# Optimization experiments

Measured on AMD Instinct MI355X. Metric: run time of the kernel, lower is better.

## Reference

```python
import jax, jax.numpy as jnp
import numpy as np

NUM_OOV = 1000
NEG = -1e12


def _lstm_cell(x, h, c, Wx, Wh, b):
    # keras gate order: i, f, g(cell), o
    z = x @ Wx + h @ Wh + b
    i, f, g, o = jnp.split(z, 4, axis=-1)
    c = jax.nn.sigmoid(f) * c + jax.nn.sigmoid(i) * jnp.tanh(g)
    h = jax.nn.sigmoid(o) * jnp.tanh(c)
    return h, c


def setup_inputs() -> dict:
    key = jax.random.key(0)
    ks = jax.random.split(key, 16)
    B, T, S, V, E, H = 16, 100, 400, 50000, 128, 256
    rn = lambda k, shp, s=0.05: (jax.random.normal(k, shp) * s).astype(jnp.float32)
    return dict(
        trg_seq=jax.random.randint(ks[0], (B, T), 0, V),
        ext_src_seq=jax.random.randint(ks[1], (B, S), 0, V + NUM_OOV),
        encoder_mask=jax.random.randint(ks[2], (B, S), 0, 2).at[:, 0].set(1),
        encoder_outputs=rn(ks[3], (B, S, H), 1.0),
        init_h=rn(ks[4], (B, H)),
        init_c=rn(ks[5], (B, H)),
        emb=rn(ks[6], (V, E)),
        W_enc=rn(ks[7], (H, H)), b_enc=jnp.zeros((H,), jnp.float32),
        W_red=rn(ks[8], (E + H, E)), b_red=jnp.zeros((E,), jnp.float32),
        Wx=rn(ks[9], (E, 4 * H)), Wh=rn(ks[10], (H, 4 * H)), b_lstm=jnp.zeros((4 * H,), jnp.float32),
        W_cat=rn(ks[11], (2 * H, H)), b_cat=jnp.zeros((H,), jnp.float32),
        W_out=rn(ks[12], (H, V)), b_out=jnp.zeros((V,), jnp.float32),
    )


def reference(trg_seq, ext_src_seq, encoder_mask, encoder_outputs, init_h, init_c,
              emb, W_enc, b_enc, W_red, b_red, Wx, Wh, b_lstm, W_cat, b_cat, W_out, b_out):
    V = W_out.shape[1]
    B, S = ext_src_seq.shape
    EXT_V = V + NUM_OOV
    memories = encoder_outputs @ W_enc + b_enc              # [B,S,H]
    mask0 = encoder_mask == 0                               # [B,S]
    bidx = jnp.arange(B)[:, None]

    def step(carry, y_t):
        h, c, ctx = carry
        x = jnp.concatenate([emb[y_t], ctx], -1) @ W_red + b_red   # [B,E]
        h, c = _lstm_cell(x, h, c, Wx, Wh, b_lstm)
        energy = jnp.einsum('bh,bsh->bs', h, memories)
        energy = jnp.where(mask0, NEG, energy)
        attn = jax.nn.softmax(energy, axis=-1)
        ctx = jnp.einsum('bs,bsh->bh', attn, memories)
        logit = jnp.tanh(jnp.concatenate([h, ctx], -1) @ W_cat + b_cat) @ W_out + b_out  # [B,V]
        ext = jnp.concatenate([logit, jnp.zeros((B, NUM_OOV), logit.dtype)], -1)         # [B,EXT_V]
        # pointer-generator copy score: per-batch scatter-max of energy over extended ids
        copy = jnp.full((B, EXT_V), NEG, logit.dtype).at[bidx, ext_src_seq].max(energy)
        copy = jnp.where(copy < NEG / 2, 0.0, copy)
        return (h, c, ctx), ext + copy

    init = (init_h, init_c, jnp.zeros_like(init_h))
    _, logits = jax.lax.scan(step, init, trg_seq.T)          # [T,B,EXT_V]
    return jnp.transpose(logits, (1, 0, 2))                  # [B,T,EXT_V]
```

## Files before the change

kernel.cpp:

```cpp
#include <hip/hip_runtime.h>

#define DEV __device__ __forceinline__

#define B_    16
#define T_    100
#define S_    400
#define V_    50000
#define EXTV  51000
#define E_    128
#define H_    256
#define H4_   1024
#define NEG_  (-1e12f)
#define NWG_  80

DEV unsigned short f2bf(float x) {
    unsigned int u = __float_as_uint(x);
    u = (u + 0x7FFFu + ((u >> 16) & 1u)) >> 16;
    return (unsigned short)u;
}
DEV float sigm(float x) { return 1.f / (1.f + __expf(-x)); }

DEV float aload(const float* p) {
    return __uint_as_float(__hip_atomic_load((const unsigned int*)p,
                           __ATOMIC_RELAXED, __HIP_MEMORY_SCOPE_AGENT));
}
DEV void astore(float* p, float v) {
    __hip_atomic_store((unsigned int*)p, __float_as_uint(v),
                       __ATOMIC_RELAXED, __HIP_MEMORY_SCOPE_AGENT);
}

DEV void gbar(int* bar, int token) {
    __syncthreads();
    const int tid = threadIdx.x;
    int* gen = bar + 1344;
    if (blockIdx.x == 0) {
        if (tid >= 1 && tid < NWG_) {
            while (__hip_atomic_load(bar + tid * 16, __ATOMIC_RELAXED,
                                     __HIP_MEMORY_SCOPE_AGENT) < token)
                __builtin_amdgcn_s_sleep(2);
        }
        __syncthreads();
        if (tid == 0)
            __hip_atomic_store(gen, token, __ATOMIC_RELAXED, __HIP_MEMORY_SCOPE_AGENT);
    } else {
        if (tid == 0) {
            __hip_atomic_store(bar + blockIdx.x * 16, token,
                               __ATOMIC_RELAXED, __HIP_MEMORY_SCOPE_AGENT);
            while (__hip_atomic_load(gen, __ATOMIC_RELAXED,
                                     __HIP_MEMORY_SCOPE_AGENT) < token)
                __builtin_amdgcn_s_sleep(2);
        }
        __syncthreads();
    }
}

__global__ void k_init(int* bar) {
    for (int i = threadIdx.x; i < 2048; i += 256) bar[i] = 0;
}


__global__ void k_mem(const float* __restrict__ enc, const float* __restrict__ W_enc,
                      const float* __restrict__ b_enc, float* __restrict__ mem) {
    __shared__ float u[16][H_];
    int base = blockIdx.x * 16;
    int j = threadIdx.x;
    for (int r = 0; r < 16; ++r) u[r][j] = enc[(base + r) * H_ + j];
    __syncthreads();
    float acc[16];
    float bb = b_enc[j];
    for (int r = 0; r < 16; ++r) acc[r] = bb;
    for (int k = 0; k < H_; ++k) {
        float wv = W_enc[k * H_ + j];
        for (int r = 0; r < 16; ++r) acc[r] = fmaf(u[r][k], wv, acc[r]);
    }
    for (int r = 0; r < 16; ++r) mem[(base + r) * H_ + j] = acc[r];
}

__global__ void k_prepw(const float* __restrict__ W_red, const float* __restrict__ Wx,
                        const float* __restrict__ Wh, const float* __restrict__ b_red,
                        const float* __restrict__ b_lstm,
                        float* __restrict__ Kt, float* __restrict__ WtW, float* __restrict__ bvec) {
    int c = blockIdx.x * 256 + threadIdx.x;
    int r = blockIdx.y;
    if (r < 384) {
        float acc = 0.f;
        for (int j = 0; j < E_; ++j) acc = fmaf(W_red[r * E_ + j], Wx[j * H4_ + c], acc);
        if (r < 128) WtW[r * H4_ + c] = acc;
        else         Kt[c * 512 + (r - 128)] = acc;
    } else if (r < 640) {
        Kt[c * 512 + 256 + (r - 384)] = Wh[(r - 384) * H4_ + c];
    } else {
        float acc = b_lstm[c];
        for (int j = 0; j < E_; ++j) acc = fmaf(b_red[j], Wx[j * H4_ + c], acc);
        bvec[c] = acc;
    }
}

__global__ void k_zpre(const int* __restrict__ trg, const float* __restrict__ emb,
                       const float* __restrict__ WtW, const float* __restrict__ bvec,
                       float* __restrict__ Zpre) {
    __shared__ float u[16][E_];
    int t = blockIdx.x, q = blockIdx.y;
    int tid = threadIdx.x;
    for (int idx = tid; idx < 16 * E_; idx += 256) {
        int b = idx >> 7, k = idx & 127;
        u[b][k] = emb[trg[b * T_ + t] * E_ + k];
    }
    __syncthreads();
    int c = q * 256 + tid;
    float acc[16];
    float bv = bvec[c];
    for (int b = 0; b < 16; ++b) acc[b] = bv;
    for (int k = 0; k < E_; ++k) {
        float wv = WtW[k * H4_ + c];
        for (int b = 0; b < 16; ++b) acc[b] = fmaf(u[b][k], wv, acc[b]);
    }
    for (int b = 0; b < 16; ++b) Zpre[(t * 16 + b) * H4_ + c] = acc[b];
}

__global__ void __launch_bounds__(512) k_loop(
    const float* __restrict__ Kt, const float* __restrict__ Zpre,
    const float* __restrict__ init_h, const float* __restrict__ init_c,
    const float* __restrict__ memw, const int* __restrict__ enc_mask,
    float* __restrict__ Mpart, float* __restrict__ Zpart, float* __restrict__ Cpart,
    float* __restrict__ ws_h, float* __restrict__ ws_ctx, float* __restrict__ ws_en,
    int* bar) {
    __shared__ __align__(16) float Kl[16 * 512];
    __shared__ __align__(16) float vL[16 * 512];
    __shared__ float zscr[16 * 17];
    __shared__ float swL[80];
    __shared__ float invd[16];
    __shared__ float hA[H_];
    __shared__ float eL[80];
    __shared__ float pL[80];
    __shared__ float red1[1];
    __shared__ float cL[512];

    const int w = blockIdx.x, tid = threadIdx.x;
    const int ub = (w & 63) << 2;

    float c_state = 0.f;
    if (w < 64 && tid < 64)
        c_state = init_c[(tid & 15) * H_ + ub + (tid >> 4)];

    if (w < 64) {
        for (int idx = tid; idx < 16 * 512; idx += 512) {
            int cs = idx >> 9, k = idx & 511;
            int col = ((cs >> 2) << 8) + ub + (cs & 3);
            Kl[idx] = Kt[col * 512 + k];
        }
    }

    for (int t = 0; ; ++t) {
        const bool aw = (t == T_) ? (w < 16) : (w < 64);
        if (aw) {
            if (t == 0) {
                for (int idx = tid; idx < 4096; idx += 512) {
                    int b = idx >> 8, k = idx & 255;
                    vL[b * 512 + k] = 0.f;
                    vL[b * 512 + 256 + k] = init_h[b * H_ + k];
                }
            } else {
                if (tid < 16) {
                    int b = tid;
                    float m[5], zp[5];
                    float M = -3.0e38f;
                    for (int i = 0; i < 5; ++i) {
                        m[i] = aload(&Mpart[i * 16 + b]); zp[i] = aload(&Zpart[i * 16 + b]);
                        M = fmaxf(M, m[i]);
                    }
                    float den = 0.f;
                    for (int i = 0; i < 5; ++i) {
                        float s = __expf(m[i] - M);
                        swL[i * 16 + b] = s;
                        den = fmaf(zp[i], s, den);
                    }
                    invd[b] = 1.f / den;
                }
                __syncthreads();
                for (int idx = tid; idx < 4096; idx += 512) {
                    int b = idx >> 8, k = idx & 255;
                    float v = 0.f;
                    for (int i = 0; i < 5; ++i)
                        v = fmaf(aload(&Cpart[(i * 16 + b) * H_ + k]), swL[i * 16 + b], v);
                    v *= invd[b];
                    vL[b * 512 + k] = v;
                    if (w == b) ws_ctx[((t - 1) * 16 + b) * H_ + k] = v;
                    vL[b * 512 + 256 + k] = aload(&ws_h[((t - 1) * 16 + b) * H_ + k]);
                }
            }
        }
        if (t == T_) break;

        if (w < 64) {
            __syncthreads();
            const int wv = tid >> 6, kl = tid & 63, k0 = kl << 3;
            for (int pass = 0; pass < 2; ++pass) {
                const int cs = pass * 8 + wv;
                const float4 kv0 = *(const float4*)(Kl + cs * 512 + k0);
                const float4 kv1 = *(const float4*)(Kl + cs * 512 + k0 + 4);
                for (int b = 0; b < 16; ++b) {
                    float4 v0 = *(const float4*)(vL + b * 512 + k0);
                    float4 v1 = *(const float4*)(vL + b * 512 + k0 + 4);
                    float acc = v0.x * kv0.x;
                    acc = fmaf(v0.y, kv0.y, acc); acc = fmaf(v0.z, kv0.z, acc);
                    acc = fmaf(v0.w, kv0.w, acc); acc = fmaf(v1.x, kv1.x, acc);
                    acc = fmaf(v1.y, kv1.y, acc); acc = fmaf(v1.z, kv1.z, acc);
                    acc = fmaf(v1.w, kv1.w, acc);
                    for (int off = 32; off; off >>= 1) acc += __shfl_xor(acc, off);
                    if (kl == 0) zscr[cs * 17 + b] = acc;
                }
            }
            __syncthreads();
            if (tid < 64) {
                const int gu = tid >> 4, gb = tid & 15;
                const float* zp2 = Zpre + (t * 16 + gb) * H4_;
                float zi = zscr[gu * 17 + gb]        + zp2[ub + gu];
                float zf = zscr[(4 + gu) * 17 + gb]  + zp2[256 + ub + gu];
                float zg = zscr[(8 + gu) * 17 + gb]  + zp2[512 + ub + gu];
                float zo = zscr[(12 + gu) * 17 + gb] + zp2[768 + ub + gu];
                float cn = sigm(zf) * c_state + sigm(zi) * tanhf(zg);
                c_state = cn;
                astore(&ws_h[(t * 16 + gb) * H_ + ub + gu], sigm(zo) * tanhf(cn));
            }
        }
        gbar(bar, 2 * t + 1);

        {
            const int bw = w & 15, sg = w >> 4;
            if (tid < H_) hA[tid] = aload(&ws_h[(t * 16 + bw) * H_ + tid]);
            __syncthreads();
            if (tid < 320) {
                const int s = tid >> 2, kq = tid & 3;
                const float* mrow = memw + (bw * S_ + sg * 80 + s) * H_ + (kq << 6);
                const float* ha = hA + (kq << 6);
                float e = 0.f;
                for (int k = 0; k < 64; k += 4) {
                    float4 mm = *(const float4*)(mrow + k);
                    e = fmaf(ha[k], mm.x, e);     e = fmaf(ha[k + 1], mm.y, e);
                    e = fmaf(ha[k + 2], mm.z, e); e = fmaf(ha[k + 3], mm.w, e);
                }
                e += __shfl_xor(e, 1);
                e += __shfl_xor(e, 2);
                if (kq == 0) {
                    if (enc_mask[bw * S_ + sg * 80 + s] == 0) e = NEG_;
                    ws_en[(t * 16 + bw) * S_ + sg * 80 + s] = e;
                    eL[s] = e;
                }
            }
            __syncthreads();
            if (tid < 64) {
                float m = eL[tid];
                if (tid < 16) m = fmaxf(m, eL[64 + tid]);
                for (int off = 32; off; off >>= 1) m = fmaxf(m, __shfl_down(m, off));
                if (tid == 0) red1[0] = m;
            }
            __syncthreads();
            const float mw = red1[0];
            if (tid < 80) pL[tid] = __expf(eL[tid] - mw);
            __syncthreads();
            if (tid < 64) {
                float zz = pL[tid] + ((tid < 16) ? pL[64 + tid] : 0.f);
                for (int off = 32; off; off >>= 1) zz += __shfl_down(zz, off);
                if (tid == 0) { astore(&Mpart[sg * 16 + bw], mw); astore(&Zpart[sg * 16 + bw], zz); }
            }
            {
                const int k = tid & 255, half = tid >> 8;
                float acc = 0.f;
                const float* mbase = memw + (bw * S_ + sg * 80) * H_;
                for (int s = half * 40; s < half * 40 + 40; ++s)
                    acc = fmaf(pL[s], mbase[s * H_ + k], acc);
                cL[tid] = acc;
                __syncthreads();
                if (tid < 256) astore(&Cpart[(sg * 16 + bw) * H_ + tid], cL[tid] + cL[tid + 256]);
            }
        }
        gbar(bar, 2 * t + 2);
    }
}


__global__ void k_precat(const float* __restrict__ ws_h, const float* __restrict__ ws_ctx,
                         const float* __restrict__ W_cat, const float* __restrict__ b_cat,
                         unsigned short* __restrict__ Abf) {
    __shared__ float u[16][512];
    int base = blockIdx.x * 16;
    int tid = threadIdx.x;
    for (int idx = tid; idx < 16 * 512; idx += 256) {
        int r = idx >> 9, k = idx & 511;
        int row = base + r;
        float v = 0.f;
        if (row < 1600) v = (k < 256) ? ws_h[row * H_ + k] : ws_ctx[row * H_ + (k - 256)];
        u[r][k] = v;
    }
    __syncthreads();
    float acc[16];
    float bc = b_cat[tid];
    for (int r = 0; r < 16; ++r) acc[r] = bc;
    for (int k = 0; k < 512; ++k) {
        float wv = W_cat[k * H_ + tid];
        for (int r = 0; r < 16; ++r) acc[r] = fmaf(u[r][k], wv, acc[r]);
    }
    for (int r = 0; r < 16; ++r) {
        int row = base + r;
        float a = (row < 1600) ? tanhf(acc[r]) : 0.f;
        Abf[row * H_ + tid] = f2bf(a);
    }
}

__global__ void k_convw(const float* __restrict__ Wout, const float* __restrict__ bout,
                        unsigned short* __restrict__ Bt, float* __restrict__ biasp) {
    __shared__ float tile[64][65];
    int bx = blockIdx.x;
    int by = blockIdx.y;
    int tid = threadIdx.x;
    int tr = tid >> 6, tc = tid & 63;
    for (int i = 0; i < 16; ++i) {
        int k = by * 64 + tr + i * 4;
        int n = bx * 64 + tc;
        tile[tr + i * 4][tc] = (n < V_) ? Wout[k * V_ + n] : 0.f;
    }
    __syncthreads();
    for (int i = 0; i < 16; ++i) {
        int nl = tr + i * 4;
        int n = bx * 64 + nl;
        int k = by * 64 + tc;
        Bt[n * 256 + k] = f2bf(tile[tc][nl]);
    }
    if (by == 0 && tid < 64) {
        int n = bx * 64 + tid;
        biasp[n] = (n < V_) ? bout[n] : 0.f;
    }
}

typedef __attribute__((ext_vector_type(8))) __bf16 bf16x8;
typedef __attribute__((ext_vector_type(4))) float f32x4;

__global__ void __launch_bounds__(256) k_gemm(
    const unsigned short* __restrict__ A, const unsigned short* __restrict__ Bt,
    const float* __restrict__ biasp, float* __restrict__ out) {
    __shared__ __align__(16) unsigned short As[128 * 64];
    __shared__ __align__(16) unsigned short Bs[128 * 64];
    const int nb = blockIdx.x, mb = blockIdx.y;
    const int tid = threadIdx.x;
    const int lane = tid & 63, wv = tid >> 6;
    const int wm = wv >> 1, wn = wv & 1;
    const int q = lane >> 4, r16 = lane & 15;
    f32x4 acc[4][4];
    for (int i = 0; i < 4; ++i) for (int j = 0; j < 4; ++j) acc[i][j] = (f32x4)0.f;
    for (int kb = 0; kb < 4; ++kb) {
        for (int i = 0; i < 4; ++i) {
            int idx = tid + (i << 8);
            int m = idx >> 3, c = idx & 7;
            int sl = ((c ^ (m & 7)) << 3);
            *(uint4*)(As + (m << 6) + sl) = *(const uint4*)(A + (mb * 128 + m) * 256 + (kb << 6) + (c << 3));
            *(uint4*)(Bs + (m << 6) + sl) = *(const uint4*)(Bt + (nb * 128 + m) * 256 + (kb << 6) + (c << 3));
        }
        __syncthreads();
        for (int k32 = 0; k32 < 2; ++k32) {
            bf16x8 af[4], bfr[4];
            int c = (k32 << 2) + q;
            for (int mt = 0; mt < 4; ++mt) {
                int m = wm * 64 + mt * 16 + r16;
                af[mt] = *(const bf16x8*)(As + (m << 6) + ((c ^ (m & 7)) << 3));
            }
            for (int nt = 0; nt < 4; ++nt) {
                int n = wn * 64 + nt * 16 + r16;
                bfr[nt] = *(const bf16x8*)(Bs + (n << 6) + ((c ^ (n & 7)) << 3));
            }
            for (int mt = 0; mt < 4; ++mt)
                for (int nt = 0; nt < 4; ++nt)
                    acc[mt][nt] = __builtin_amdgcn_mfma_f32_16x16x32_bf16(af[mt], bfr[nt], acc[mt][nt], 0, 0, 0);
        }
        __syncthreads();
    }
    for (int nt = 0; nt < 4; ++nt) {
        int col = nb * 128 + wn * 64 + nt * 16 + r16;
        if (col >= EXTV) continue;
        float bs = biasp[col];
        for (int mt = 0; mt < 4; ++mt) {
            int rbase = mb * 128 + wm * 64 + mt * 16 + (q << 2);
            for (int rg = 0; rg < 4; ++rg) {
                int row = rbase + rg;
                if (row < 1600) {
                    int tt = row >> 4, bb = row & 15;
                    out[(bb * T_ + tt) * EXTV + col] = acc[mt][nt][rg] + bs;
                }
            }
        }
    }
}

__global__ void k_scatter(const int* __restrict__ ext_ids, const float* __restrict__ ws_en,
                          float* __restrict__ out) {
    __shared__ int ids[S_];
    __shared__ float en[S_];
    int r = blockIdx.x;
    int t = r >> 4, b = r & 15;
    int tid = threadIdx.x;
    for (int s = tid; s < S_; s += 256) {
        ids[s] = ext_ids[b * S_ + s];
        en[s] = ws_en[r * S_ + s];
    }
    __syncthreads();
    for (int s = tid; s < S_; s += 256) {
        int id = ids[s];
        float mx = en[s];
        int fo = s;
        for (int s2 = 0; s2 < S_; ++s2) {
            if (ids[s2] == id) { mx = fmaxf(mx, en[s2]); if (s2 < fo) fo = s2; }
        }
        if (fo == s && mx >= NEG_ * 0.5f)
            out[(b * T_ + t) * EXTV + id] += mx;
    }
}


extern "C" void kernel_launch(void* const* d_in, const int* in_sizes, int n_in,
                              void* d_out, int out_size, void* d_ws, size_t ws_size,
                              hipStream_t stream) {
    (void)in_sizes; (void)n_in; (void)out_size; (void)ws_size;
    const int*   trg     = (const int*)d_in[0];
    const int*   ext_ids = (const int*)d_in[1];
    const int*   mask    = (const int*)d_in[2];
    const float* enc     = (const float*)d_in[3];
    const float* init_h  = (const float*)d_in[4];
    const float* init_c  = (const float*)d_in[5];
    const float* emb     = (const float*)d_in[6];
    const float* W_enc   = (const float*)d_in[7];
    const float* b_enc   = (const float*)d_in[8];
    const float* W_red   = (const float*)d_in[9];
    const float* b_red   = (const float*)d_in[10];
    const float* Wx      = (const float*)d_in[11];
    const float* Wh      = (const float*)d_in[12];
    const float* b_lstm  = (const float*)d_in[13];
    const float* W_cat   = (const float*)d_in[14];
    const float* b_cat   = (const float*)d_in[15];
    const float* W_out   = (const float*)d_in[16];
    const float* b_out   = (const float*)d_in[17];
    float* out = (float*)d_out;

    char* p = (char*)d_ws;
    auto alloc = [&](size_t bytes) { char* r = p; p += ((bytes + 255) & ~size_t(255)); return r; };
    float* mem_w = (float*)alloc(1638400u * 4);
    float* Kt    = (float*)alloc(524288u * 4);
    float* WtW   = (float*)alloc(131072u * 4);
    float* bvec  = (float*)alloc(1024u * 4);
    float* Zpre  = (float*)alloc(1638400u * 4);
    float* Mpart = (float*)alloc(128u * 4);
    float* Zpart = (float*)alloc(128u * 4);
    float* Cpart = (float*)alloc(20480u * 4);
    float* ws_h  = (float*)alloc(409600u * 4);
    float* ws_ctx= (float*)alloc(409600u * 4);
    float* ws_en = (float*)alloc(640000u * 4);
    unsigned short* Abf = (unsigned short*)alloc(425984u * 2);
    unsigned short* Bt  = (unsigned short*)alloc(13074432u * 2);
    float* biasp = (float*)alloc(51072u * 4);
    int* bar = (int*)alloc(2048u * 4);

    k_init<<<dim3(1), dim3(256), 0, stream>>>(bar);
    k_mem<<<dim3(400), dim3(256), 0, stream>>>(enc, W_enc, b_enc, mem_w);
    k_prepw<<<dim3(4, 641), dim3(256), 0, stream>>>(W_red, Wx, Wh, b_red, b_lstm, Kt, WtW, bvec);
    k_zpre<<<dim3(100, 4), dim3(256), 0, stream>>>(trg, emb, WtW, bvec, Zpre);

    k_loop<<<dim3(NWG_), dim3(512), 0, stream>>>(Kt, Zpre, init_h, init_c, mem_w, mask,
                                                 Mpart, Zpart, Cpart, ws_h, ws_ctx, ws_en, bar);

    k_precat<<<dim3(104), dim3(256), 0, stream>>>(ws_h, ws_ctx, W_cat, b_cat, Abf);
    k_convw<<<dim3(798, 4), dim3(256), 0, stream>>>(W_out, b_out, Bt, biasp);
    k_gemm<<<dim3(399, 13), dim3(256), 0, stream>>>(Abf, Bt, biasp, out);
    k_scatter<<<dim3(1600), dim3(256), 0, stream>>>(ext_ids, ws_en, out);
}
```

Measured before the change: 2.774 ms.

## Use all-to-all flag barrier and 64-bit atomic transfers in recurrent loop

Replaces the centralized grid barrier, where block 0 gathers arrivals and then broadcasts a generation flag, with a flat barrier in which every block publishes its own flag and polls all 80 flags directly. This removes one round-trip of latency per barrier. It also switches the cross-block exchanges of h, context partials and ws_h reads to 64-bit relaxed atomics, which halves the number of atomic memory operations. The new barrier adds more polling traffic, with 80 flags read by each block, and relies on an explicit vmcnt wait for ordering. An unused buffer allocation is also added.

```diff
diff --git a/kernel.cpp b/kernel.cpp
--- a/kernel.cpp
+++ b/kernel.cpp
@@ -28,30 +28,30 @@
     __hip_atomic_store((unsigned int*)p, __float_as_uint(v),
                        __ATOMIC_RELAXED, __HIP_MEMORY_SCOPE_AGENT);
 }
+DEV float2 aload64(const float* p) {
+    unsigned long long v = __hip_atomic_load((const unsigned long long*)p,
+                           __ATOMIC_RELAXED, __HIP_MEMORY_SCOPE_AGENT);
+    float2 f; __builtin_memcpy(&f, &v, 8); return f;
+}
+DEV void astore64(float* p, float a, float b) {
+    float2 f; f.x = a; f.y = b;
+    unsigned long long v; __builtin_memcpy(&v, &f, 8);
+    __hip_atomic_store((unsigned long long*)p, v,
+                       __ATOMIC_RELAXED, __HIP_MEMORY_SCOPE_AGENT);
+}
 
 DEV void gbar(int* bar, int token) {
+    asm volatile("s_waitcnt vmcnt(0)" ::: "memory");
     __syncthreads();
     const int tid = threadIdx.x;
-    int* gen = bar + 1344;
-    if (blockIdx.x == 0) {
-        if (tid >= 1 && tid < NWG_) {
-            while (__hip_atomic_load(bar + tid * 16, __ATOMIC_RELAXED,
-                                     __HIP_MEMORY_SCOPE_AGENT) < token)
-                __builtin_amdgcn_s_sleep(2);
-        }
-        __syncthreads();
-        if (tid == 0)
-            __hip_atomic_store(gen, token, __ATOMIC_RELAXED, __HIP_MEMORY_SCOPE_AGENT);
-    } else {
-        if (tid == 0) {
-            __hip_atomic_store(bar + blockIdx.x * 16, token,
-                               __ATOMIC_RELAXED, __HIP_MEMORY_SCOPE_AGENT);
-            while (__hip_atomic_load(gen, __ATOMIC_RELAXED,
-                                     __HIP_MEMORY_SCOPE_AGENT) < token)
-                __builtin_amdgcn_s_sleep(2);
-        }
-        __syncthreads();
-    }
+    if (tid == (int)blockIdx.x)
+        __hip_atomic_store(bar + tid * 16, token, __ATOMIC_RELAXED, __HIP_MEMORY_SCOPE_AGENT);
+    if (tid < NWG_) {
+        while (__hip_atomic_load(bar + tid * 16, __ATOMIC_RELAXED,
+                                 __HIP_MEMORY_SCOPE_AGENT) < token)
+            __builtin_amdgcn_s_sleep(1);
+    }
+    __syncthreads();
 }
 
 __global__ void k_init(int* bar) {
@@ -130,6 +130,7 @@
     __shared__ float zscr[16 * 17];
     __shared__ float swL[80];
     __shared__ float invd[16];
+    __shared__ float hstage[64];
     __shared__ float hA[H_];
     __shared__ float eL[80];
     __shared__ float pL[80];
@@ -178,15 +179,23 @@
                     invd[b] = 1.f / den;
                 }
                 __syncthreads();
-                for (int idx = tid; idx < 4096; idx += 512) {
-                    int b = idx >> 8, k = idx & 255;
-                    float v = 0.f;
-                    for (int i = 0; i < 5; ++i)
-                        v = fmaf(aload(&Cpart[(i * 16 + b) * H_ + k]), swL[i * 16 + b], v);
-                    v *= invd[b];
-                    vL[b * 512 + k] = v;
-                    if (w == b) ws_ctx[((t - 1) * 16 + b) * H_ + k] = v;
-                    vL[b * 512 + 256 + k] = aload(&ws_h[((t - 1) * 16 + b) * H_ + k]);
+                for (int pr = tid; pr < 2048; pr += 512) {
+                    int b = pr >> 7, kp = (pr & 127) << 1;
+                    float v0 = 0.f, v1 = 0.f;
+                    for (int i = 0; i < 5; ++i) {
+                        float2 cc = aload64(&Cpart[(i * 16 + b) * H_ + kp]);
+                        float s = swL[i * 16 + b];
+                        v0 = fmaf(cc.x, s, v0); v1 = fmaf(cc.y, s, v1);
+                    }
+                    float iv = invd[b];
+                    v0 *= iv; v1 *= iv;
+                    vL[b * 512 + kp] = v0; vL[b * 512 + kp + 1] = v1;
+                    if (w == b) {
+                        ws_ctx[((t - 1) * 16 + b) * H_ + kp] = v0;
+                        ws_ctx[((t - 1) * 16 + b) * H_ + kp + 1] = v1;
+                    }
+                    float2 hh = aload64(&ws_h[((t - 1) * 16 + b) * H_ + kp]);
+                    vL[b * 512 + 256 + kp] = hh.x; vL[b * 512 + 256 + kp + 1] = hh.y;
                 }
             }
         }
@@ -221,14 +230,23 @@
                 float zo = zscr[(12 + gu) * 17 + gb] + zp2[768 + ub + gu];
                 float cn = sigm(zf) * c_state + sigm(zi) * tanhf(zg);
                 c_state = cn;
-                astore(&ws_h[(t * 16 + gb) * H_ + ub + gu], sigm(zo) * tanhf(cn));
+                hstage[gb * 4 + gu] = sigm(zo) * tanhf(cn);
+            }
+            __syncthreads();
+            if (tid < 32) {
+                int gb = tid >> 1, j = tid & 1;
+                astore64(&ws_h[(t * 16 + gb) * H_ + ub + j * 2],
+                         hstage[gb * 4 + j * 2], hstage[gb * 4 + j * 2 + 1]);
             }
         }
         gbar(bar, 2 * t + 1);
 
         {
             const int bw = w & 15, sg = w >> 4;
-            if (tid < H_) hA[tid] = aload(&ws_h[(t * 16 + bw) * H_ + tid]);
+            if (tid < 128) {
+                float2 hh = aload64(&ws_h[(t * 16 + bw) * H_ + tid * 2]);
+                hA[tid * 2] = hh.x; hA[tid * 2 + 1] = hh.y;
+            }
             __syncthreads();
             if (tid < 320) {
                 const int s = tid >> 2, kq = tid & 3;
@@ -272,7 +290,10 @@
                     acc = fmaf(pL[s], mbase[s * H_ + k], acc);
                 cL[tid] = acc;
                 __syncthreads();
-                if (tid < 256) astore(&Cpart[(sg * 16 + bw) * H_ + tid], cL[tid] + cL[tid + 256]);
+                if (tid < 256) cL[tid] += cL[tid + 256];
+                __syncthreads();
+                if (tid < 128)
+                    astore64(&Cpart[(sg * 16 + bw) * H_ + tid * 2], cL[tid * 2], cL[tid * 2 + 1]);
             }
         }
         gbar(bar, 2 * t + 2);
@@ -450,6 +471,7 @@
     float* Mpart = (float*)alloc(128u * 4);
     float* Zpart = (float*)alloc(128u * 4);
     float* Cpart = (float*)alloc(20480u * 4);
+    float* cbuf  = (float*)alloc(4096u * 4);
     float* ws_h  = (float*)alloc(409600u * 4);
     float* ws_ctx= (float*)alloc(409600u * 4);
     float* ws_en = (float*)alloc(640000u * 4);
@@ -457,6 +479,7 @@
     unsigned short* Bt  = (unsigned short*)alloc(13074432u * 2);
     float* biasp = (float*)alloc(51072u * 4);
     int* bar = (int*)alloc(2048u * 4);
+    (void)cbuf;
 
     k_init<<<dim3(1), dim3(256), 0, stream>>>(bar);
     k_mem<<<dim3(400), dim3(256), 0, stream>>>(enc, W_enc, b_enc, mem_w);
```

Result: no change. 2.779 ms (+0.2%).
